# Optimization experiments

Measured on AMD Instinct MI355X. Metric: run time of the kernel, lower is better.

The kernel has to match this reference:

```python
import jax, jax.numpy as jnp
import numpy as np

S = 32        # num_subdomains
D = 1         # in_size
WIDTH = 128   # width_size
DEPTH = 4     # eqx MLP depth -> 1 input layer + (DEPTH-1) hidden layers + 1 output layer
N = 262144    # collocation points
TOL = 1e-8


def setup_inputs() -> dict:
    key = jax.random.key(0)
    ks = jax.random.split(key, 7)
    # subdomain i = [(i-0.5)/S, (i+1.5)/S] -> center (i+0.5)/S, half-width 1/S
    centers = ((jnp.arange(S, dtype=jnp.float32) + 0.5) / S)[:, None]          # (S, D)
    scales = jnp.full((S, D), 1.0 / S, dtype=jnp.float32)                       # (S, D)

    def unif(k, shape, fan_in):  # equinox Linear init: U(-1/sqrt(fan_in), 1/sqrt(fan_in))
        lim = 1.0 / np.sqrt(fan_in)
        return jax.random.uniform(k, shape, jnp.float32, -lim, lim)

    W_in = unif(ks[0], (S, WIDTH, D), D)
    b_in = unif(ks[1], (S, WIDTH), D)
    W_hid = unif(ks[2], (S, DEPTH - 1, WIDTH, WIDTH), WIDTH)
    b_hid = unif(ks[3], (S, DEPTH - 1, WIDTH), WIDTH)
    W_out = unif(ks[4], (S, 1, WIDTH), WIDTH)
    b_out = unif(ks[5], (S, 1), WIDTH)
    x = jax.random.uniform(ks[6], (N, D), jnp.float32, 0.0, 1.0)
    return {"x": x, "W_in": W_in, "b_in": b_in, "W_hid": W_hid, "b_hid": b_hid,
            "W_out": W_out, "b_out": b_out, "centers": centers, "scales": scales}


def reference(x, W_in, b_in, W_hid, b_hid, W_out, b_out, centers, scales):
    # normalized coords per subdomain: (S, n, D)
    u = (x[None, :, :] - centers[:, None, :]) / scales[:, None, :]
    # partition-of-unity cosine window, product over dims, normalized over subdomains
    raw = jnp.prod(jnp.where(jnp.abs(u) < 1.0, jnp.cos(0.5 * jnp.pi * u) ** 2, 0.0), axis=-1)  # (S, n)
    w = raw / (jnp.sum(raw, axis=0, keepdims=True) + TOL)                                       # (S, n)

    def body(total, p):
        Wi, bi, Wh, bh, Wo, bo, xn, wk = p
        h = jnp.tanh(xn @ Wi.T + bi)                      # (n, WIDTH)
        for l in range(DEPTH - 1):                        # static unroll over hidden layers
            h = jnp.tanh(h @ Wh[l].T + bh[l])
        out = (h @ Wo.T + bo)[:, 0]                       # (n,)
        return total + wk * out, None

    total, _ = jax.lax.scan(body, jnp.zeros(x.shape[0], x.dtype),
                            (W_in, b_in, W_hid, b_hid, W_out, b_out, u, w))
    # ansatz = identity
    return total
```

## Files before the change

kernel.cpp:

```cpp
#include <hip/hip_runtime.h>

#define NS 32
#define WID 128
#define NHID 3
#define NPTS 262144
#define PTILE 256
#define TMLP 512
#define CAP 17408
#define TPB (CAP / PTILE)

#define TASKS_OFF 512
#define WF_OFF (TASKS_OFF + NS * CAP * 4)
#define TANH_C 2.8853900817779268f

typedef _Float16 f16x2 __attribute__((ext_vector_type(2)));
typedef _Float16 f16x4 __attribute__((ext_vector_type(4)));
typedef _Float16 f16x8 __attribute__((ext_vector_type(8)));
typedef __fp16 fp16x2 __attribute__((ext_vector_type(2)));
typedef float f32x4 __attribute__((ext_vector_type(4)));

union U4H8 { uint4 u; f16x8 h; };
union PK2 { fp16x2 p; f16x2 h; };
union H4U2 { f16x4 h; uint2 u; };

__device__ __forceinline__ f16x2 pk2(float a, float b) {
    PK2 u; u.p = __builtin_amdgcn_cvt_pkrtz(a, b); return u.h;
}

__device__ __forceinline__ float tanh_fast(float v) {
    float a = v * TANH_C;
    float e; asm("v_exp_f32 %0, %1" : "=v"(e) : "v"(a));
    float d = e + 1.0f;
    float r; asm("v_rcp_f32 %0, %1" : "=v"(r) : "v"(d));
    return fmaf(-2.0f, r, 1.0f);
}

__device__ __forceinline__ float tanh_pre(float a) {
    float e; asm("v_exp_f32 %0, %1" : "=v"(e) : "v"(a));
    float d = e + 1.0f;
    float r; asm("v_rcp_f32 %0, %1" : "=v"(r) : "v"(d));
    return fmaf(-2.0f, r, 1.0f);
}

__device__ __forceinline__ float coswin(float u) {
    if (fabsf(u) >= 1.0f) return 0.0f;
    float rev = u * 0.25f;
    float c; asm("v_cos_f32 %0, %1" : "=v"(c) : "v"(rev));
    return c * c;
}


__global__ __launch_bounds__(256) void k_prep(
    const float* __restrict__ Wh, uint4* __restrict__ WfU4,
    const float* __restrict__ x, int* __restrict__ cursors,
    int* __restrict__ tasks, float* __restrict__ out, int n) {
    __shared__ _Float16 sW[128 * 132];
    __shared__ int loc[NS];
    __shared__ int base[NS];
    const int b = blockIdx.x;
    const int t = threadIdx.x;
    if (b < 96) {
        const float* src = Wh + (size_t)b * 16384;
#pragma unroll
        for (int it = 0; it < 16; ++it) {
            int idx = it * 1024 + t * 4;
            int o = idx >> 7, c = idx & 127;
            float4 v = *(const float4*)(src + idx);
            f16x4 hv;
            hv[0] = (_Float16)(v.x * TANH_C);
            hv[1] = (_Float16)(v.y * TANH_C);
            hv[2] = (_Float16)(v.z * TANH_C);
            hv[3] = (_Float16)(v.w * TANH_C);
            *(f16x4*)&sW[o * 132 + c] = hv;
        }
        __syncthreads();
#pragma unroll
        for (int it = 0; it < 8; ++it) {
            int f = it * 256 + t;
            int lane = f & 63, s = (f >> 6) & 3, t8 = f >> 8;
            int o = 16 * t8 + (lane & 15), h = lane >> 4;
            H4U2 lo, hi;
            lo.h = *(f16x4*)&sW[o * 132 + 32 * s + 4 * h];
            hi.h = *(f16x4*)&sW[o * 132 + 32 * s + 4 * h + 16];
            uint4 outv = {lo.u.x, lo.u.y, hi.u.x, hi.u.y};
            WfU4[(size_t)b * 2048 + f] = outv;
        }
    } else {
        if (t < NS) loc[t] = 0;
        __syncthreads();
        int i = (b - 96) * 256 + t;
        int j = -1, nb = -1, sj = 0, snb = 0;
        if (i < n) {
            out[i] = 0.0f;
            float tt = x[i] * 32.0f;
            j = min(max((int)floorf(tt), 0), 31);
            sj = atomicAdd(&loc[j], 1);
            float u = tt - (float)j - 0.5f;
            int nb2 = (u > 0.0f) ? j + 1 : j - 1;
            if (u != 0.0f && nb2 >= 0 && nb2 < NS) { nb = nb2; snb = atomicAdd(&loc[nb], 1); }
        }
        __syncthreads();
        if (t < NS) base[t] = atomicAdd(&cursors[t], loc[t]);
        __syncthreads();
        if (i < n) {
            tasks[j * CAP + base[j] + sj] = i;
            if (nb >= 0) tasks[nb * CAP + base[nb] + snb] = i;
        }
    }
}


__global__ __launch_bounds__(TMLP, 4) void k_mlp(
    const float* __restrict__ x, const float* __restrict__ W_in, const float* __restrict__ b_in,
    const float* __restrict__ b_hid, const float* __restrict__ W_out, const float* __restrict__ b_out,
    const float* __restrict__ centers, const float* __restrict__ scales,
    const int* __restrict__ cursors, const int* __restrict__ tasks,
    const uint4* __restrict__ WfU4, float* __restrict__ out) {

    const int bin = blockIdx.y;
    const int tile = blockIdx.x;
    const int cnt = cursors[bin];
    if (tile * PTILE >= cnt) return;
    const int start = bin * CAP;

    __shared__ __align__(256) _Float16 HT[8][4096];
    __shared__ float lU[PTILE], lWgt[PTILE];
    __shared__ int lTid[PTILE];

    const int t = threadIdx.x;
    const int lane = t & 63;
    const int l15 = t & 15;
    const int g = (t >> 4) & 3;
    const int w = t >> 6;

    if (t < PTILE) {
        int idx = tile * PTILE + t;
        if (idx < cnt) {
            int pid = tasks[start + idx];
            lTid[t] = pid;
            float xx = x[pid];
            float u = (xx - centers[bin]) * (1.0f / scales[bin]);
            lU[t] = u;
            float rs = coswin(u);
            int other = bin + (u > 0.0f ? 1 : -1);
            float ro = 0.0f;
            if (other >= 0 && other < NS)
                ro = coswin((xx - centers[other]) * (1.0f / scales[other]));
            lWgt[t] = rs / (rs + ro + 1e-8f);
        } else { lTid[t] = -1; lU[t] = 0.0f; lWgt[t] = 0.0f; }
    }
    __syncthreads();

    const uint4* wfbase = WfU4 + (size_t)(bin * NHID) * 32 * 64 + lane;

    uint4 bufA[4], bufB[4];
#pragma unroll
    for (int s = 0; s < 4; ++s) bufA[s] = wfbase[s * 64];

    {
        float4 ua = *(const float4*)&lU[w * 32 + 4 * g];
        float4 ub = *(const float4*)&lU[w * 32 + 16 + 4 * g];
        const float* Win = W_in + bin * WID;
        const float* Bi  = b_in + bin * WID;
#pragma unroll
        for (int t8 = 0; t8 < 8; ++t8) {
            int o = 16 * t8 + l15;
            float wv = Win[o], bv = Bi[o];
            f16x2 h00 = pk2(tanh_fast(fmaf(ua.x, wv, bv)), tanh_fast(fmaf(ua.y, wv, bv)));
            f16x2 h01 = pk2(tanh_fast(fmaf(ua.z, wv, bv)), tanh_fast(fmaf(ua.w, wv, bv)));
            f16x2 h10 = pk2(tanh_fast(fmaf(ub.x, wv, bv)), tanh_fast(fmaf(ub.y, wv, bv)));
            f16x2 h11 = pk2(tanh_fast(fmaf(ub.z, wv, bv)), tanh_fast(fmaf(ub.w, wv, bv)));
            *(f16x4*)&HT[w][o * 16 + 4 * g] = __builtin_shufflevector(h00, h01, 0, 1, 2, 3);
            *(f16x4*)&HT[w][2048 + o * 16 + 4 * g] = __builtin_shufflevector(h10, h11, 0, 1, 2, 3);
        }
    }

    const unsigned htaddr = (unsigned)(size_t)&HT[w][0] + lane * 8;
    float p0 = 0.f, p1 = 0.f, p2 = 0.f, p3 = 0.f;
    float q0 = 0.f, q1 = 0.f, q2 = 0.f, q3 = 0.f;

#pragma unroll
    for (int lyr = 0; lyr < NHID; ++lyr) {
        f16x4 r0, r1, r2, r3, r4, r5, r6, r7, r8, r9, r10, r11, r12, r13, r14, r15;
        asm volatile(
            "ds_read_b64_tr_b16 %0, %16 offset:0\n\t"
            "ds_read_b64_tr_b16 %1, %16 offset:512\n\t"
            "ds_read_b64_tr_b16 %2, %16 offset:1024\n\t"
            "ds_read_b64_tr_b16 %3, %16 offset:1536\n\t"
            "ds_read_b64_tr_b16 %4, %16 offset:2048\n\t"
            "ds_read_b64_tr_b16 %5, %16 offset:2560\n\t"
            "ds_read_b64_tr_b16 %6, %16 offset:3072\n\t"
            "ds_read_b64_tr_b16 %7, %16 offset:3584\n\t"
            "ds_read_b64_tr_b16 %8, %16 offset:4096\n\t"
            "ds_read_b64_tr_b16 %9, %16 offset:4608\n\t"
            "ds_read_b64_tr_b16 %10, %16 offset:5120\n\t"
            "ds_read_b64_tr_b16 %11, %16 offset:5632\n\t"
            "ds_read_b64_tr_b16 %12, %16 offset:6144\n\t"
            "ds_read_b64_tr_b16 %13, %16 offset:6656\n\t"
            "ds_read_b64_tr_b16 %14, %16 offset:7168\n\t"
            "ds_read_b64_tr_b16 %15, %16 offset:7680\n\t"
            "s_waitcnt lgkmcnt(0)"
            : "=v"(r0), "=v"(r1), "=v"(r2), "=v"(r3), "=v"(r4), "=v"(r5), "=v"(r6), "=v"(r7),
              "=v"(r8), "=v"(r9), "=v"(r10), "=v"(r11), "=v"(r12), "=v"(r13), "=v"(r14), "=v"(r15)
            : "v"(htaddr) : "memory");
        f16x8 A0[4], A1[4];
        A0[0] = __builtin_shufflevector(r0, r1, 0, 1, 2, 3, 4, 5, 6, 7);
        A0[1] = __builtin_shufflevector(r2, r3, 0, 1, 2, 3, 4, 5, 6, 7);
        A0[2] = __builtin_shufflevector(r4, r5, 0, 1, 2, 3, 4, 5, 6, 7);
        A0[3] = __builtin_shufflevector(r6, r7, 0, 1, 2, 3, 4, 5, 6, 7);
        A1[0] = __builtin_shufflevector(r8, r9, 0, 1, 2, 3, 4, 5, 6, 7);
        A1[1] = __builtin_shufflevector(r10, r11, 0, 1, 2, 3, 4, 5, 6, 7);
        A1[2] = __builtin_shufflevector(r12, r13, 0, 1, 2, 3, 4, 5, 6, 7);
        A1[3] = __builtin_shufflevector(r14, r15, 0, 1, 2, 3, 4, 5, 6, 7);

        const float* bh = b_hid + (size_t)(bin * NHID + lyr) * WID;
        float bhv[8];
#pragma unroll
        for (int t8 = 0; t8 < 8; ++t8) bhv[t8] = bh[16 * t8 + l15] * TANH_C;

        const uint4* wfL = wfbase + (size_t)lyr * 32 * 64;
        const uint4* wfN = wfbase + (size_t)(lyr + 1) * 32 * 64;

#pragma unroll
        for (int tp = 0; tp < 4; ++tp) {
            const int t8a = 2 * tp, t8b = 2 * tp + 1;
#pragma unroll
            for (int s = 0; s < 4; ++s) bufB[s] = wfL[(t8b * 4 + s) * 64];

            f32x4 acc0 = (f32x4){0.f, 0.f, 0.f, 0.f};
            f32x4 acc1 = (f32x4){0.f, 0.f, 0.f, 0.f};
            __builtin_amdgcn_s_setprio(1);
#pragma unroll
            for (int s = 0; s < 4; ++s) {
                U4H8 bw; bw.u = bufA[s];
                acc0 = __builtin_amdgcn_mfma_f32_16x16x32_f16(A0[s], bw.h, acc0, 0, 0, 0);
                acc1 = __builtin_amdgcn_mfma_f32_16x16x32_f16(A1[s], bw.h, acc1, 0, 0, 0);
            }
            __builtin_amdgcn_s_setprio(0);

            if (lyr < NHID - 1) {
                int o = 16 * t8a + l15;
                float bv = bhv[t8a];
                f16x2 h00 = pk2(tanh_pre(acc0[0] + bv), tanh_pre(acc0[1] + bv));
                f16x2 h01 = pk2(tanh_pre(acc0[2] + bv), tanh_pre(acc0[3] + bv));
                f16x2 h10 = pk2(tanh_pre(acc1[0] + bv), tanh_pre(acc1[1] + bv));
                f16x2 h11 = pk2(tanh_pre(acc1[2] + bv), tanh_pre(acc1[3] + bv));
                *(f16x4*)&HT[w][o * 16 + 4 * g] = __builtin_shufflevector(h00, h01, 0, 1, 2, 3);
                *(f16x4*)&HT[w][2048 + o * 16 + 4 * g] = __builtin_shufflevector(h10, h11, 0, 1, 2, 3);
            } else {
                float bv = bhv[t8a], wv = W_out[bin * WID + 16 * t8a + l15];
                p0 = fmaf(wv, tanh_pre(acc0[0] + bv), p0);
                p1 = fmaf(wv, tanh_pre(acc0[1] + bv), p1);
                p2 = fmaf(wv, tanh_pre(acc0[2] + bv), p2);
                p3 = fmaf(wv, tanh_pre(acc0[3] + bv), p3);
                q0 = fmaf(wv, tanh_pre(acc1[0] + bv), q0);
                q1 = fmaf(wv, tanh_pre(acc1[1] + bv), q1);
                q2 = fmaf(wv, tanh_pre(acc1[2] + bv), q2);
                q3 = fmaf(wv, tanh_pre(acc1[3] + bv), q3);
            }

            if (t8b < 7) {
#pragma unroll
                for (int s = 0; s < 4; ++s) bufA[s] = wfL[((t8b + 1) * 4 + s) * 64];
            } else if (lyr < NHID - 1) {
#pragma unroll
                for (int s = 0; s < 4; ++s) bufA[s] = wfN[s * 64];
            }

            f32x4 bcc0 = (f32x4){0.f, 0.f, 0.f, 0.f};
            f32x4 bcc1 = (f32x4){0.f, 0.f, 0.f, 0.f};
            __builtin_amdgcn_s_setprio(1);
#pragma unroll
            for (int s = 0; s < 4; ++s) {
                U4H8 bw; bw.u = bufB[s];
                bcc0 = __builtin_amdgcn_mfma_f32_16x16x32_f16(A0[s], bw.h, bcc0, 0, 0, 0);
                bcc1 = __builtin_amdgcn_mfma_f32_16x16x32_f16(A1[s], bw.h, bcc1, 0, 0, 0);
            }
            __builtin_amdgcn_s_setprio(0);

            if (lyr < NHID - 1) {
                int o = 16 * t8b + l15;
                float bv = bhv[t8b];
                f16x2 h00 = pk2(tanh_pre(bcc0[0] + bv), tanh_pre(bcc0[1] + bv));
                f16x2 h01 = pk2(tanh_pre(bcc0[2] + bv), tanh_pre(bcc0[3] + bv));
                f16x2 h10 = pk2(tanh_pre(bcc1[0] + bv), tanh_pre(bcc1[1] + bv));
                f16x2 h11 = pk2(tanh_pre(bcc1[2] + bv), tanh_pre(bcc1[3] + bv));
                *(f16x4*)&HT[w][o * 16 + 4 * g] = __builtin_shufflevector(h00, h01, 0, 1, 2, 3);
                *(f16x4*)&HT[w][2048 + o * 16 + 4 * g] = __builtin_shufflevector(h10, h11, 0, 1, 2, 3);
            } else {
                float bv = bhv[t8b], wv = W_out[bin * WID + 16 * t8b + l15];
                p0 = fmaf(wv, tanh_pre(bcc0[0] + bv), p0);
                p1 = fmaf(wv, tanh_pre(bcc0[1] + bv), p1);
                p2 = fmaf(wv, tanh_pre(bcc0[2] + bv), p2);
                p3 = fmaf(wv, tanh_pre(bcc0[3] + bv), p3);
                q0 = fmaf(wv, tanh_pre(bcc1[0] + bv), q0);
                q1 = fmaf(wv, tanh_pre(bcc1[1] + bv), q1);
                q2 = fmaf(wv, tanh_pre(bcc1[2] + bv), q2);
                q3 = fmaf(wv, tanh_pre(bcc1[3] + bv), q3);
            }
        }
    }

#pragma unroll
    for (int m = 1; m < 16; m <<= 1) {
        p0 += __shfl_xor(p0, m); p1 += __shfl_xor(p1, m);
        p2 += __shfl_xor(p2, m); p3 += __shfl_xor(p3, m);
        q0 += __shfl_xor(q0, m); q1 += __shfl_xor(q1, m);
        q2 += __shfl_xor(q2, m); q3 += __shfl_xor(q3, m);
    }
    if (l15 < 4) {
        float bo = b_out[bin];
        float v0 = ((l15 == 0) ? p0 : (l15 == 1) ? p1 : (l15 == 2) ? p2 : p3) + bo;
        float v1 = ((l15 == 0) ? q0 : (l15 == 1) ? q1 : (l15 == 2) ? q2 : q3) + bo;
        int pl0 = w * 32 + 4 * g + l15;
        int pl1 = pl0 + 16;
        int pid0 = lTid[pl0], pid1 = lTid[pl1];
        if (pid0 >= 0) atomicAdd(out + pid0, lWgt[pl0] * v0);
        if (pid1 >= 0) atomicAdd(out + pid1, lWgt[pl1] * v1);
    }
}

extern "C" void kernel_launch(void* const* d_in, const int* in_sizes, int n_in,
                              void* d_out, int out_size, void* d_ws, size_t ws_size,
                              hipStream_t stream) {
    const float* x       = (const float*)d_in[0];
    const float* W_in    = (const float*)d_in[1];
    const float* b_in    = (const float*)d_in[2];
    const float* W_hid   = (const float*)d_in[3];
    const float* b_hid   = (const float*)d_in[4];
    const float* W_out   = (const float*)d_in[5];
    const float* b_out   = (const float*)d_in[6];
    const float* centers = (const float*)d_in[7];
    const float* scales  = (const float*)d_in[8];
    float* out = (float*)d_out;

    char* ws = (char*)d_ws;
    int* cursors = (int*)(ws);
    int* tasks   = (int*)(ws + TASKS_OFF);
    uint4* WfU4  = (uint4*)(ws + WF_OFF);

    (void)hipMemsetAsync(ws, 0, 256, stream);

    k_prep<<<dim3(96 + NPTS / 256), dim3(256), 0, stream>>>(W_hid, WfU4, x, cursors,
                                                            tasks, out, NPTS);
    k_mlp<<<dim3(TPB, NS), dim3(TMLP), 0, stream>>>(x, W_in, b_in, b_hid, W_out, b_out,
                                                    centers, scales, cursors, tasks,
                                                    WfU4, out);
}
```

Measured before the change: 113.3 us.

## Software-pipeline weight loads with inline asm and stage per-bin params in LDS

Replaces the compiler-scheduled double-buffered weight fetches with hand-issued global_load_dwordx4 groups into two register buffers. Explicit vmcnt waits keep one chunk in flight while MFMAs consume the other, and sched_barriers pin the ordering. Per-bin small parameters (W_in, b_in, pre-scaled b_hid, W_out, b_out) are loaded once into shared memory by the otherwise idle upper threads instead of being re-read from global memory inside the loops. This risks fragile manual vmcnt accounting and adds a little LDS use and scheduling rigidity.

```diff
diff --git a/kernel.cpp b/kernel.cpp
--- a/kernel.cpp
+++ b/kernel.cpp
@@ -48,6 +48,14 @@
     float c; asm("v_cos_f32 %0, %1" : "=v"(c) : "v"(rev));
     return c * c;
 }
+
+#define ISSUE4(B, A)                                                     \
+    asm volatile(                                                        \
+        "global_load_dwordx4 %0, %4, off\n\t"                            \
+        "global_load_dwordx4 %1, %4, off offset:1024\n\t"                \
+        "global_load_dwordx4 %2, %4, off offset:2048\n\t"                \
+        "global_load_dwordx4 %3, %4, off offset:3072"                    \
+        : "=&v"(B[0]), "=&v"(B[1]), "=&v"(B[2]), "=&v"(B[3]) : "v"(A))
 
 
 __global__ __launch_bounds__(256) void k_prep(
@@ -126,6 +134,7 @@
     __shared__ __align__(256) _Float16 HT[8][4096];
     __shared__ float lU[PTILE], lWgt[PTILE];
     __shared__ int lTid[PTILE];
+    __shared__ float sPar[769];
 
     const int t = threadIdx.x;
     const int lane = t & 63;
@@ -148,24 +157,33 @@
                 ro = coswin((xx - centers[other]) * (1.0f / scales[other]));
             lWgt[t] = rs / (rs + ro + 1e-8f);
         } else { lTid[t] = -1; lU[t] = 0.0f; lWgt[t] = 0.0f; }
+    } else {
+        int j = t - 256;
+#pragma unroll
+        for (int r = 0; r < 3; ++r) {
+            int ii = r * 256 + j;
+            if (ii < 128)        sPar[ii] = W_in[bin * WID + ii];
+            else if (ii < 256)   sPar[ii] = b_in[bin * WID + ii - 128];
+            else if (ii < 640)   sPar[ii] = b_hid[bin * 384 + ii - 256] * TANH_C;
+            else if (ii < 768)   sPar[ii] = W_out[bin * WID + ii - 640];
+        }
+        if (j == 255) sPar[768] = b_out[bin];
     }
     __syncthreads();
 
-    const uint4* wfbase = WfU4 + (size_t)(bin * NHID) * 32 * 64 + lane;
-
-    uint4 bufA[4], bufB[4];
-#pragma unroll
-    for (int s = 0; s < 4; ++s) bufA[s] = wfbase[s * 64];
+    unsigned long long wfa = (unsigned long long)(WfU4 + (size_t)(bin * NHID) * 2048)
+                           + (unsigned long long)(lane) * 16ull;
+    uint4 B0[4], B1[4];
+    ISSUE4(B0, wfa); wfa += 4096;
+    ISSUE4(B1, wfa); wfa += 4096;
 
     {
         float4 ua = *(const float4*)&lU[w * 32 + 4 * g];
         float4 ub = *(const float4*)&lU[w * 32 + 16 + 4 * g];
-        const float* Win = W_in + bin * WID;
-        const float* Bi  = b_in + bin * WID;
 #pragma unroll
         for (int t8 = 0; t8 < 8; ++t8) {
             int o = 16 * t8 + l15;
-            float wv = Win[o], bv = Bi[o];
+            float wv = sPar[o], bv = sPar[128 + o];
             f16x2 h00 = pk2(tanh_fast(fmaf(ua.x, wv, bv)), tanh_fast(fmaf(ua.y, wv, bv)));
             f16x2 h01 = pk2(tanh_fast(fmaf(ua.z, wv, bv)), tanh_fast(fmaf(ua.w, wv, bv)));
             f16x2 h10 = pk2(tanh_fast(fmaf(ub.x, wv, bv)), tanh_fast(fmaf(ub.y, wv, bv)));
@@ -203,6 +221,7 @@
             : "=v"(r0), "=v"(r1), "=v"(r2), "=v"(r3), "=v"(r4), "=v"(r5), "=v"(r6), "=v"(r7),
               "=v"(r8), "=v"(r9), "=v"(r10), "=v"(r11), "=v"(r12), "=v"(r13), "=v"(r14), "=v"(r15)
             : "v"(htaddr) : "memory");
+        __builtin_amdgcn_sched_barrier(0);
         f16x8 A0[4], A1[4];
         A0[0] = __builtin_shufflevector(r0, r1, 0, 1, 2, 3, 4, 5, 6, 7);
         A0[1] = __builtin_shufflevector(r2, r3, 0, 1, 2, 3, 4, 5, 6, 7);
@@ -213,34 +232,35 @@
         A1[2] = __builtin_shufflevector(r12, r13, 0, 1, 2, 3, 4, 5, 6, 7);
         A1[3] = __builtin_shufflevector(r14, r15, 0, 1, 2, 3, 4, 5, 6, 7);
 
-        const float* bh = b_hid + (size_t)(bin * NHID + lyr) * WID;
-        float bhv[8];
-#pragma unroll
-        for (int t8 = 0; t8 < 8; ++t8) bhv[t8] = bh[16 * t8 + l15] * TANH_C;
-
-        const uint4* wfL = wfbase + (size_t)lyr * 32 * 64;
-        const uint4* wfN = wfbase + (size_t)(lyr + 1) * 32 * 64;
-
-#pragma unroll
-        for (int tp = 0; tp < 4; ++tp) {
-            const int t8a = 2 * tp, t8b = 2 * tp + 1;
-#pragma unroll
-            for (int s = 0; s < 4; ++s) bufB[s] = wfL[(t8b * 4 + s) * 64];
+#pragma unroll
+        for (int t8 = 0; t8 < 8; ++t8) {
+            const int i = lyr * 8 + t8;
+            if (i < 23) asm volatile("s_waitcnt vmcnt(4)" ::: "memory");
+            else        asm volatile("s_waitcnt vmcnt(0)" ::: "memory");
+            __builtin_amdgcn_sched_barrier(0);
 
             f32x4 acc0 = (f32x4){0.f, 0.f, 0.f, 0.f};
             f32x4 acc1 = (f32x4){0.f, 0.f, 0.f, 0.f};
             __builtin_amdgcn_s_setprio(1);
 #pragma unroll
             for (int s = 0; s < 4; ++s) {
-                U4H8 bw; bw.u = bufA[s];
+                U4H8 bw;
+                bw.u = (i % 2 == 0) ? B0[s] : B1[s];
                 acc0 = __builtin_amdgcn_mfma_f32_16x16x32_f16(A0[s], bw.h, acc0, 0, 0, 0);
                 acc1 = __builtin_amdgcn_mfma_f32_16x16x32_f16(A1[s], bw.h, acc1, 0, 0, 0);
             }
             __builtin_amdgcn_s_setprio(0);
-
+            __builtin_amdgcn_sched_barrier(0);
+
+            if (i < 22) {
+                if (i % 2 == 0) { ISSUE4(B0, wfa); }
+                else            { ISSUE4(B1, wfa); }
+                wfa += 4096;
+            }
+
+            float bv = sPar[256 + lyr * 128 + 16 * t8 + l15];
             if (lyr < NHID - 1) {
-                int o = 16 * t8a + l15;
-                float bv = bhv[t8a];
+                int o = 16 * t8 + l15;
                 f16x2 h00 = pk2(tanh_pre(acc0[0] + bv), tanh_pre(acc0[1] + bv));
                 f16x2 h01 = pk2(tanh_pre(acc0[2] + bv), tanh_pre(acc0[3] + bv));
                 f16x2 h10 = pk2(tanh_pre(acc1[0] + bv), tanh_pre(acc1[1] + bv));
@@ -248,7 +268,7 @@
                 *(f16x4*)&HT[w][o * 16 + 4 * g] = __builtin_shufflevector(h00, h01, 0, 1, 2, 3);
                 *(f16x4*)&HT[w][2048 + o * 16 + 4 * g] = __builtin_shufflevector(h10, h11, 0, 1, 2, 3);
             } else {
-                float bv = bhv[t8a], wv = W_out[bin * WID + 16 * t8a + l15];
+                float wv = sPar[640 + 16 * t8 + l15];
                 p0 = fmaf(wv, tanh_pre(acc0[0] + bv), p0);
                 p1 = fmaf(wv, tanh_pre(acc0[1] + bv), p1);
                 p2 = fmaf(wv, tanh_pre(acc0[2] + bv), p2);
@@ -258,46 +278,6 @@
                 q2 = fmaf(wv, tanh_pre(acc1[2] + bv), q2);
                 q3 = fmaf(wv, tanh_pre(acc1[3] + bv), q3);
             }
-
-            if (t8b < 7) {
-#pragma unroll
-                for (int s = 0; s < 4; ++s) bufA[s] = wfL[((t8b + 1) * 4 + s) * 64];
-            } else if (lyr < NHID - 1) {
-#pragma unroll
-                for (int s = 0; s < 4; ++s) bufA[s] = wfN[s * 64];
-            }
-
-            f32x4 bcc0 = (f32x4){0.f, 0.f, 0.f, 0.f};
-            f32x4 bcc1 = (f32x4){0.f, 0.f, 0.f, 0.f};
-            __builtin_amdgcn_s_setprio(1);
-#pragma unroll
-            for (int s = 0; s < 4; ++s) {
-                U4H8 bw; bw.u = bufB[s];
-                bcc0 = __builtin_amdgcn_mfma_f32_16x16x32_f16(A0[s], bw.h, bcc0, 0, 0, 0);
-                bcc1 = __builtin_amdgcn_mfma_f32_16x16x32_f16(A1[s], bw.h, bcc1, 0, 0, 0);
-            }
-            __builtin_amdgcn_s_setprio(0);
-
-            if (lyr < NHID - 1) {
-                int o = 16 * t8b + l15;
-                float bv = bhv[t8b];
-                f16x2 h00 = pk2(tanh_pre(bcc0[0] + bv), tanh_pre(bcc0[1] + bv));
-                f16x2 h01 = pk2(tanh_pre(bcc0[2] + bv), tanh_pre(bcc0[3] + bv));
-                f16x2 h10 = pk2(tanh_pre(bcc1[0] + bv), tanh_pre(bcc1[1] + bv));
-                f16x2 h11 = pk2(tanh_pre(bcc1[2] + bv), tanh_pre(bcc1[3] + bv));
-                *(f16x4*)&HT[w][o * 16 + 4 * g] = __builtin_shufflevector(h00, h01, 0, 1, 2, 3);
-                *(f16x4*)&HT[w][2048 + o * 16 + 4 * g] = __builtin_shufflevector(h10, h11, 0, 1, 2, 3);
-            } else {
-                float bv = bhv[t8b], wv = W_out[bin * WID + 16 * t8b + l15];
-                p0 = fmaf(wv, tanh_pre(bcc0[0] + bv), p0);
-                p1 = fmaf(wv, tanh_pre(bcc0[1] + bv), p1);
-                p2 = fmaf(wv, tanh_pre(bcc0[2] + bv), p2);
-                p3 = fmaf(wv, tanh_pre(bcc0[3] + bv), p3);
-                q0 = fmaf(wv, tanh_pre(bcc1[0] + bv), q0);
-                q1 = fmaf(wv, tanh_pre(bcc1[1] + bv), q1);
-                q2 = fmaf(wv, tanh_pre(bcc1[2] + bv), q2);
-                q3 = fmaf(wv, tanh_pre(bcc1[3] + bv), q3);
-            }
         }
     }
 
@@ -309,7 +289,7 @@
         q2 += __shfl_xor(q2, m); q3 += __shfl_xor(q3, m);
     }
     if (l15 < 4) {
-        float bo = b_out[bin];
+        float bo = sPar[768];
         float v0 = ((l15 == 0) ? p0 : (l15 == 1) ? p1 : (l15 == 2) ? p2 : p3) + bo;
         float v1 = ((l15 == 0) ? q0 : (l15 == 1) ? q1 : (l15 == 2) ? q2 : q3) + bo;
         int pl0 = w * 32 + 4 * g + l15;
```

Measured after the change: 112.5 us. No clear change (-0.8%).
